# Kernel optimization log

Hardware: AMD Instinct MI355X
Metric: run time of the kernel (lower is better)

The kernel has to match this reference:

```python
import jax, jax.numpy as jnp
import numpy as np

N_NODES = 62      # config.note_num (SEED EEG electrodes)
BATCH   = 1024    # graphs per batch
IN_CH   = 5
HID     = 64
OUT_CH  = 3
K_HOPS  = 2       # config.K


def setup_inputs() -> dict:
    key = jax.random.key(0)
    ks = jax.random.split(key, 8)
    total = BATCH * N_NODES
    x = jax.random.normal(ks[0], (total, IN_CH), dtype=jnp.float32)
    # fully-connected per-graph edge_index in row-major order (incl. self-loops),
    # matching edge_weight.reshape(-1).repeat(batch_size) in the torch code
    src = jnp.repeat(jnp.arange(N_NODES, dtype=jnp.int32), N_NODES)
    dst = jnp.tile(jnp.arange(N_NODES, dtype=jnp.int32), N_NODES)
    offs = (jnp.arange(BATCH, dtype=jnp.int32) * N_NODES)[:, None]
    edge_index = jnp.stack([
        (src[None, :] + offs).reshape(-1),
        (dst[None, :] + offs).reshape(-1),
    ])  # [2, BATCH*3844]
    batch = jnp.repeat(jnp.arange(BATCH, dtype=jnp.int32), N_NODES)
    n_tril = N_NODES * (N_NODES + 1) // 2  # 1953
    edge_weight_param = jax.random.normal(ks[1], (n_tril,), dtype=jnp.float32)
    w1 = jax.random.normal(ks[2], (HID, IN_CH), dtype=jnp.float32) * (1.0 / np.sqrt(IN_CH))
    b1 = jnp.zeros((HID,), dtype=jnp.float32)
    w2 = jax.random.normal(ks[3], (HID, HID), dtype=jnp.float32) * (1.0 / np.sqrt(HID))
    b2 = jnp.zeros((HID,), dtype=jnp.float32)
    wfc = jax.random.normal(ks[4], (OUT_CH, HID), dtype=jnp.float32) * (1.0 / np.sqrt(HID))
    bfc = jnp.zeros((OUT_CH,), dtype=jnp.float32)
    return dict(x=x, edge_index=edge_index, batch=batch,
                edge_weight_param=edge_weight_param,
                w1=w1, b1=b1, w2=w2, b2=b2, wfc=wfc, bfc=bfc)


def _gcn_norm(edge_index, edge_weight, num_nodes):
    # Graph already contains every self-loop, so add_remaining_self_loops only
    # reorders edges; normalization math is identical on the original edge set.
    row, col = edge_index[0], edge_index[1]
    deg = jax.ops.segment_sum(jnp.abs(edge_weight), row, num_segments=num_nodes)
    deg_inv_sqrt = jnp.where(deg > 0, jax.lax.rsqrt(deg), 0.0)
    return deg_inv_sqrt[row] * edge_weight * deg_inv_sqrt[col]


def _rsgconv(x, src, dst, norm, w, b):
    n = x.shape[0]
    for _ in range(K_HOPS):  # K propagation hops (gather-scale-scatter)
        x = jax.ops.segment_sum(norm[:, None] * x[src], dst, num_segments=n)
    return x @ w.T + b


def reference(x, edge_index, batch, edge_weight_param, w1, b1, w2, b2, wfc, bfc):
    num_nodes = x.shape[0]
    # rebuild symmetric dense 62x62 edge-weight matrix from learnable tril vector
    xs, ys = jnp.tril_indices(N_NODES)
    W = jnp.zeros((N_NODES, N_NODES), dtype=x.dtype).at[xs, ys].set(edge_weight_param)
    W = W + W.T - jnp.diag(jnp.diag(W))
    edge_weight = jnp.tile(W.reshape(-1), BATCH)  # [BATCH*3844]
    norm = _gcn_norm(edge_index, edge_weight, num_nodes)
    src, dst = edge_index[0], edge_index[1]
    h = jax.nn.relu(_rsgconv(x, src, dst, norm, w1, b1))
    h = jax.nn.relu(_rsgconv(h, src, dst, norm, w2, b2))
    pooled = jax.ops.segment_sum(h, batch, num_segments=BATCH)  # global_add_pool
    # dropout is identity in eval mode
    return pooled @ wfc.T + bfc
```

## Files before the change

### kernel.cpp

```cpp
#include <hip/hip_runtime.h>

#define NN 62
#define NP 64
#define NBATCH 1024
#define IN_CH 5
#define HID 64
#define OUT_CH 3
#define NTRIL 1953
#define H1S 72
#define GS 17

typedef _Float16 f16;
typedef f16 half8 __attribute__((ext_vector_type(8)));
typedef float floatx4 __attribute__((ext_vector_type(4)));

__global__ __launch_bounds__(64) void setup_k(const float* __restrict__ p,
                                              const float* __restrict__ w2,
                                              f16* __restrict__ a2h,
                                              f16* __restrict__ a2l,
                                              f16* __restrict__ w2h,
                                              f16* __restrict__ w2l) {
    __shared__ float sA[NN * NP];
    __shared__ float sDinv[NN];
    const int lane = threadIdx.x;
    const int n = blockIdx.x;

    {
        float wv = w2[n * HID + lane];
        f16 wh = (f16)wv;
        w2h[n * NP + lane] = wh;
        w2l[n * NP + lane] = (f16)(wv - (float)wh);
    }

    for (int i = lane; i < NN * NP; i += 64) sA[i] = 0.f;
    __syncthreads();

    for (int i = lane; i < NTRIL; i += 64) {
        int r = (int)((sqrtf(8.f * (float)i + 1.f) - 1.f) * 0.5f);
        while (r * (r + 1) / 2 > i) --r;
        while ((r + 1) * (r + 2) / 2 <= i) ++r;
        int c = i - r * (r + 1) / 2;
        float v = p[i];
        sA[r * NP + c] = v;
        sA[c * NP + r] = v;
    }
    __syncthreads();

    if (lane < NN) {
        float s = 0.f;
        for (int j = 0; j < NN; ++j) s += fabsf(sA[lane * NP + j]);
        sDinv[lane] = (s > 0.f) ? (1.0f / sqrtf(s)) : 0.f;
    }
    __syncthreads();

    for (int i = lane; i < NN * NP; i += 64) {
        int r = i >> 6, c = i & 63;
        float dc = (c < NN) ? sDinv[c] : 0.f;
        sA[i] = sDinv[r] * sA[i] * dc;
    }
    __syncthreads();

    float acc = 0.f;
    if (n < NN)
        for (int k = 0; k < NN; ++k) acc += sA[n * NP + k] * sA[k * NP + lane];
    f16 ah = (f16)acc;
    a2h[n * NP + lane] = ah;
    a2l[n * NP + lane] = (f16)(acc - (float)ah);
}

__global__ __launch_bounds__(256, 4) void graph_net(
    const float* __restrict__ x,
    const f16* __restrict__ a2h, const f16* __restrict__ a2l,
    const f16* __restrict__ w2h, const f16* __restrict__ w2l,
    const float* __restrict__ w1, const float* __restrict__ b1,
    const float* __restrict__ b2,
    const float* __restrict__ wfc, const float* __restrict__ bfc,
    float* __restrict__ out) {
    __shared__ __align__(16) char smem[37120];
    f16* sUTh = (f16*)smem;
    f16* sUTl = (f16*)(smem + 9216);
    float* sG  = (float*)smem;
    f16* sH1h = (f16*)(smem + 18432);
    f16* sH1l = (f16*)(smem + 27648);
    float* sPool = (float*)(smem + 36864);

    const int t = threadIdx.x;
    const int lane = t & 63;
    const int w = __builtin_amdgcn_readfirstlane(t >> 6);
    const int g = blockIdx.x;
    const float* xg = x + (size_t)g * (NN * IN_CH);

    const int jn = lane & 15;
    const int qd = lane >> 4;
    const int jglob = 16 * w + jn;

    half8 aFh[4][2], aFl[4][2];
#pragma unroll
    for (int T = 0; T < 4; ++T)
#pragma unroll
        for (int ks = 0; ks < 2; ++ks) {
            aFh[T][ks] = *(const half8*)(a2h + (16 * T + jn) * NP + qd * 8 + 32 * ks);
            aFl[T][ks] = *(const half8*)(a2l + (16 * T + jn) * NP + qd * 8 + 32 * ks);
        }

    int xi[IN_CH];
    {
        const int L = (lane < NN) ? lane : (NN - 1);
        const int* xgi = (const int*)xg;
#pragma unroll
        for (int c = 0; c < IN_CH; ++c) xi[c] = xgi[L * IN_CH + c];
    }
    float w1r[IN_CH];
#pragma unroll
    for (int c = 0; c < IN_CH; ++c) w1r[c] = w1[lane * IN_CH + c];

#pragma unroll
    for (int ni = 0; ni < 16; ++ni) {
        const int n = 16 * w + ni;
        if (n < NN) {
            float u = 0.f;
#pragma unroll
            for (int c = 0; c < IN_CH; ++c)
                u += __int_as_float(__builtin_amdgcn_readlane(xi[c], n)) * w1r[c];
            f16 uh = (f16)u;
            sUTh[lane * H1S + n] = uh;
            sUTl[lane * H1S + n] = (f16)(u - (float)uh);
        }
    }
    if (t < 128) {
        const int n = 62 + (t >> 6);
        sUTh[(t & 63) * H1S + n] = (f16)0.f;
        sUTl[(t & 63) * H1S + n] = (f16)0.f;
    }
    __syncthreads();

    half8 bUh[2], bUl[2];
#pragma unroll
    for (int ks = 0; ks < 2; ++ks) {
        bUh[ks] = *(const half8*)(sUTh + jglob * H1S + qd * 8 + 32 * ks);
        bUl[ks] = *(const half8*)(sUTl + jglob * H1S + qd * 8 + 32 * ks);
    }
    floatx4 C1[4];
#pragma unroll
    for (int T = 0; T < 4; ++T) { C1[T][0]=0.f; C1[T][1]=0.f; C1[T][2]=0.f; C1[T][3]=0.f; }
#pragma unroll
    for (int T = 0; T < 4; ++T) {
#pragma unroll
        for (int ks = 0; ks < 2; ++ks) {
            C1[T] = __builtin_amdgcn_mfma_f32_16x16x32_f16(aFl[T][ks], bUh[ks], C1[T], 0, 0, 0);
            C1[T] = __builtin_amdgcn_mfma_f32_16x16x32_f16(aFh[T][ks], bUl[ks], C1[T], 0, 0, 0);
            C1[T] = __builtin_amdgcn_mfma_f32_16x16x32_f16(aFh[T][ks], bUh[ks], C1[T], 0, 0, 0);
        }
    }
    {
        const float b1r = b1[jglob];
#pragma unroll
        for (int T = 0; T < 4; ++T)
#pragma unroll
            for (int r = 0; r < 4; ++r) {
                const int n = 16 * T + qd * 4 + r;
                float v = fmaxf(C1[T][r] + b1r, 0.f);
                f16 vh = (f16)v;
                sH1h[n * H1S + jglob] = vh;
                sH1l[n * H1S + jglob] = (f16)(v - (float)vh);
            }
    }
    __syncthreads();

    half8 bWh[2], bWl[2];
#pragma unroll
    for (int ks = 0; ks < 2; ++ks) {
        bWh[ks] = *(const half8*)(w2h + jglob * NP + qd * 8 + 32 * ks);
        bWl[ks] = *(const half8*)(w2l + jglob * NP + qd * 8 + 32 * ks);
    }
    floatx4 Cg[4];
#pragma unroll
    for (int T = 0; T < 4; ++T) { Cg[T][0]=0.f; Cg[T][1]=0.f; Cg[T][2]=0.f; Cg[T][3]=0.f; }
#pragma unroll
    for (int T = 0; T < 4; ++T) {
#pragma unroll
        for (int ks = 0; ks < 2; ++ks) {
            const half8 aH = *(const half8*)(sH1h + (16 * T + jn) * H1S + qd * 8 + 32 * ks);
            const half8 aL = *(const half8*)(sH1l + (16 * T + jn) * H1S + qd * 8 + 32 * ks);
            Cg[T] = __builtin_amdgcn_mfma_f32_16x16x32_f16(aL, bWh[ks], Cg[T], 0, 0, 0);
            Cg[T] = __builtin_amdgcn_mfma_f32_16x16x32_f16(aH, bWl[ks], Cg[T], 0, 0, 0);
            Cg[T] = __builtin_amdgcn_mfma_f32_16x16x32_f16(aH, bWh[ks], Cg[T], 0, 0, 0);
        }
    }
    {
        float* gw = sG + w * (NP * GS);
#pragma unroll
        for (int T = 0; T < 4; ++T)
#pragma unroll
            for (int r = 0; r < 4; ++r)
                gw[(16 * T + qd * 4 + r) * GS + jn] = Cg[T][r];
    }
    __syncthreads();

    half8 bGh[2], bGl[2];
    {
        const float* gr = sG + w * (NP * GS);
#pragma unroll
        for (int ks = 0; ks < 2; ++ks)
#pragma unroll
            for (int i = 0; i < 8; ++i) {
                float v = gr[(qd * 8 + i + 32 * ks) * GS + jn];
                f16 vh = (f16)v;
                bGh[ks][i] = vh;
                bGl[ks][i] = (f16)(v - (float)vh);
            }
    }

    floatx4 C2[4];
#pragma unroll
    for (int T = 0; T < 4; ++T) { C2[T][0]=0.f; C2[T][1]=0.f; C2[T][2]=0.f; C2[T][3]=0.f; }
#pragma unroll
    for (int T = 0; T < 4; ++T) {
#pragma unroll
        for (int ks = 0; ks < 2; ++ks) {
            C2[T] = __builtin_amdgcn_mfma_f32_16x16x32_f16(aFl[T][ks], bGh[ks], C2[T], 0, 0, 0);
            C2[T] = __builtin_amdgcn_mfma_f32_16x16x32_f16(aFh[T][ks], bGl[ks], C2[T], 0, 0, 0);
            C2[T] = __builtin_amdgcn_mfma_f32_16x16x32_f16(aFh[T][ks], bGh[ks], C2[T], 0, 0, 0);
        }
    }

    {
        const float b2r = b2[jglob];
        float pool = 0.f;
#pragma unroll
        for (int T = 0; T < 4; ++T)
#pragma unroll
            for (int r = 0; r < 4; ++r) {
                const int n = 16 * T + qd * 4 + r;
                float v = fmaxf(C2[T][r] + b2r, 0.f);
                pool += (n < NN) ? v : 0.f;
            }
        pool += __shfl_xor(pool, 16);
        pool += __shfl_xor(pool, 32);
        if (lane < 16) sPool[jglob] = pool;
    }
    __syncthreads();

    if (t < OUT_CH) {
        float v = bfc[t];
        const float* wr = wfc + t * HID;
#pragma unroll
        for (int m = 0; m < HID; ++m) v += sPool[m] * wr[m];
        out[g * OUT_CH + t] = v;
    }
}

extern "C" void kernel_launch(void* const* d_in, const int* in_sizes, int n_in,
                              void* d_out, int out_size, void* d_ws, size_t ws_size,
                              hipStream_t stream) {
    const float* x   = (const float*)d_in[0];
    const float* ewp = (const float*)d_in[3];
    const float* w1  = (const float*)d_in[4];
    const float* b1  = (const float*)d_in[5];
    const float* w2  = (const float*)d_in[6];
    const float* b2  = (const float*)d_in[7];
    const float* wfc = (const float*)d_in[8];
    const float* bfc = (const float*)d_in[9];
    float* out = (float*)d_out;

    f16* a2h = (f16*)d_ws;
    f16* a2l = a2h + NP * NP;
    f16* w2h = a2l + NP * NP;
    f16* w2l = w2h + NP * NP;

    setup_k<<<NP, 64, 0, stream>>>(ewp, w2, a2h, a2l, w2h, w2l);
    graph_net<<<NBATCH, 256, 0, stream>>>(x, a2h, a2l, w2h, w2l,
                                          w1, b1, b2, wfc, bfc, out);
}
```

Baseline: 123.3 us.

## Compute first-layer x·W1 projection with MFMA and drop block-wide barriers

Replaces the scalar readlane-based x·W1ᵀ projection with split-f16 MFMA ops, for which W1 is pre-split into hi/lo halves in the setup kernel. The result goes through a per-wave shared-memory scratch region instead of a block-shared transpose buffer. Because each wave now only reads back its own slice, two __syncthreads barriers are removed and shared memory shrinks slightly. This adds 12 MFMAs that are mostly zero padding (K=5 padded to 32), in exchange for removing the serial readlane loop and the block synchronisation.

```diff
diff --git a/kernel.cpp b/kernel.cpp
--- a/kernel.cpp
+++ b/kernel.cpp
@@ -16,10 +16,13 @@
 
 __global__ __launch_bounds__(64) void setup_k(const float* __restrict__ p,
                                               const float* __restrict__ w2,
+                                              const float* __restrict__ w1,
                                               f16* __restrict__ a2h,
                                               f16* __restrict__ a2l,
                                               f16* __restrict__ w2h,
-                                              f16* __restrict__ w2l) {
+                                              f16* __restrict__ w2l,
+                                              f16* __restrict__ w1h,
+                                              f16* __restrict__ w1l) {
     __shared__ float sA[NN * NP];
     __shared__ float sDinv[NN];
     const int lane = threadIdx.x;
@@ -30,6 +33,12 @@
         f16 wh = (f16)wv;
         w2h[n * NP + lane] = wh;
         w2l[n * NP + lane] = (f16)(wv - (float)wh);
+    }
+    if (lane < 8) {
+        float wv = (lane < IN_CH) ? w1[n * IN_CH + lane] : 0.f;
+        f16 wh = (f16)wv;
+        w1h[n * 8 + lane] = wh;
+        w1l[n * 8 + lane] = (f16)(wv - (float)wh);
     }
 
     for (int i = lane; i < NN * NP; i += 64) sA[i] = 0.f;
@@ -72,17 +81,15 @@
     const float* __restrict__ x,
     const f16* __restrict__ a2h, const f16* __restrict__ a2l,
     const f16* __restrict__ w2h, const f16* __restrict__ w2l,
-    const float* __restrict__ w1, const float* __restrict__ b1,
-    const float* __restrict__ b2,
+    const f16* __restrict__ w1h, const f16* __restrict__ w1l,
+    const float* __restrict__ b1, const float* __restrict__ b2,
     const float* __restrict__ wfc, const float* __restrict__ bfc,
     float* __restrict__ out) {
-    __shared__ __align__(16) char smem[37120];
-    f16* sUTh = (f16*)smem;
-    f16* sUTl = (f16*)(smem + 9216);
-    float* sG  = (float*)smem;
-    f16* sH1h = (f16*)(smem + 18432);
-    f16* sH1l = (f16*)(smem + 27648);
-    float* sPool = (float*)(smem + 36864);
+    __shared__ __align__(16) char smem[36096];
+    float* sPG = (float*)smem;
+    f16* sH1h = (f16*)(smem + 17408);
+    f16* sH1l = (f16*)(smem + 26624);
+    float* sPool = (float*)(smem + 35840);
 
     const int t = threadIdx.x;
     const int lane = t & 63;
@@ -93,6 +100,7 @@
     const int jn = lane & 15;
     const int qd = lane >> 4;
     const int jglob = 16 * w + jn;
+    float* gw = sPG + w * (NP * GS);
 
     half8 aFh[4][2], aFl[4][2];
 #pragma unroll
@@ -103,43 +111,53 @@
             aFl[T][ks] = *(const half8*)(a2l + (16 * T + jn) * NP + qd * 8 + 32 * ks);
         }
 
-    int xi[IN_CH];
-    {
-        const int L = (lane < NN) ? lane : (NN - 1);
-        const int* xgi = (const int*)xg;
-#pragma unroll
-        for (int c = 0; c < IN_CH; ++c) xi[c] = xgi[L * IN_CH + c];
-    }
-    float w1r[IN_CH];
-#pragma unroll
-    for (int c = 0; c < IN_CH; ++c) w1r[c] = w1[lane * IN_CH + c];
-
-#pragma unroll
-    for (int ni = 0; ni < 16; ++ni) {
-        const int n = 16 * w + ni;
-        if (n < NN) {
-            float u = 0.f;
-#pragma unroll
-            for (int c = 0; c < IN_CH; ++c)
-                u += __int_as_float(__builtin_amdgcn_readlane(xi[c], n)) * w1r[c];
-            f16 uh = (f16)u;
-            sUTh[lane * H1S + n] = uh;
-            sUTl[lane * H1S + n] = (f16)(u - (float)uh);
-        }
-    }
-    if (t < 128) {
-        const int n = 62 + (t >> 6);
-        sUTh[(t & 63) * H1S + n] = (f16)0.f;
-        sUTl[(t & 63) * H1S + n] = (f16)0.f;
-    }
-    __syncthreads();
-
+    half8 aXh[4], aXl[4];
+#pragma unroll
+    for (int T = 0; T < 4; ++T) {
+        half8 hx = (half8)(f16)0.f, lx = (half8)(f16)0.f;
+        const int n = 16 * T + jn;
+        if (qd == 0 && n < NN) {
+            const float* xr = xg + n * IN_CH;
+#pragma unroll
+            for (int c = 0; c < IN_CH; ++c) {
+                float v = xr[c];
+                f16 vh = (f16)v;
+                hx[c] = vh;
+                lx[c] = (f16)(v - (float)vh);
+            }
+        }
+        aXh[T] = hx; aXl[T] = lx;
+    }
+    half8 bW1h = (half8)(f16)0.f, bW1l = (half8)(f16)0.f;
+    if (qd == 0) {
+        bW1h = *(const half8*)(w1h + jglob * 8);
+        bW1l = *(const half8*)(w1l + jglob * 8);
+    }
+    floatx4 P[4];
+#pragma unroll
+    for (int T = 0; T < 4; ++T) { P[T][0]=0.f; P[T][1]=0.f; P[T][2]=0.f; P[T][3]=0.f; }
+#pragma unroll
+    for (int T = 0; T < 4; ++T) {
+        P[T] = __builtin_amdgcn_mfma_f32_16x16x32_f16(aXl[T], bW1h, P[T], 0, 0, 0);
+        P[T] = __builtin_amdgcn_mfma_f32_16x16x32_f16(aXh[T], bW1l, P[T], 0, 0, 0);
+        P[T] = __builtin_amdgcn_mfma_f32_16x16x32_f16(aXh[T], bW1h, P[T], 0, 0, 0);
+    }
+#pragma unroll
+    for (int T = 0; T < 4; ++T)
+#pragma unroll
+        for (int r = 0; r < 4; ++r)
+            gw[(16 * T + qd * 4 + r) * GS + jn] = P[T][r];
     half8 bUh[2], bUl[2];
 #pragma unroll
-    for (int ks = 0; ks < 2; ++ks) {
-        bUh[ks] = *(const half8*)(sUTh + jglob * H1S + qd * 8 + 32 * ks);
-        bUl[ks] = *(const half8*)(sUTl + jglob * H1S + qd * 8 + 32 * ks);
-    }
+    for (int ks = 0; ks < 2; ++ks)
+#pragma unroll
+        for (int i = 0; i < 8; ++i) {
+            float v = gw[(qd * 8 + i + 32 * ks) * GS + jn];
+            f16 vh = (f16)v;
+            bUh[ks][i] = vh;
+            bUl[ks][i] = (f16)(v - (float)vh);
+        }
+
     floatx4 C1[4];
 #pragma unroll
     for (int T = 0; T < 4; ++T) { C1[T][0]=0.f; C1[T][1]=0.f; C1[T][2]=0.f; C1[T][3]=0.f; }
@@ -187,29 +205,21 @@
             Cg[T] = __builtin_amdgcn_mfma_f32_16x16x32_f16(aH, bWh[ks], Cg[T], 0, 0, 0);
         }
     }
-    {
-        float* gw = sG + w * (NP * GS);
-#pragma unroll
-        for (int T = 0; T < 4; ++T)
-#pragma unroll
-            for (int r = 0; r < 4; ++r)
-                gw[(16 * T + qd * 4 + r) * GS + jn] = Cg[T][r];
-    }
-    __syncthreads();
-
+#pragma unroll
+    for (int T = 0; T < 4; ++T)
+#pragma unroll
+        for (int r = 0; r < 4; ++r)
+            gw[(16 * T + qd * 4 + r) * GS + jn] = Cg[T][r];
     half8 bGh[2], bGl[2];
-    {
-        const float* gr = sG + w * (NP * GS);
-#pragma unroll
-        for (int ks = 0; ks < 2; ++ks)
-#pragma unroll
-            for (int i = 0; i < 8; ++i) {
-                float v = gr[(qd * 8 + i + 32 * ks) * GS + jn];
-                f16 vh = (f16)v;
-                bGh[ks][i] = vh;
-                bGl[ks][i] = (f16)(v - (float)vh);
-            }
-    }
+#pragma unroll
+    for (int ks = 0; ks < 2; ++ks)
+#pragma unroll
+        for (int i = 0; i < 8; ++i) {
+            float v = gw[(qd * 8 + i + 32 * ks) * GS + jn];
+            f16 vh = (f16)v;
+            bGh[ks][i] = vh;
+            bGl[ks][i] = (f16)(v - (float)vh);
+        }
 
     floatx4 C2[4];
 #pragma unroll
@@ -267,8 +277,10 @@
     f16* a2l = a2h + NP * NP;
     f16* w2h = a2l + NP * NP;
     f16* w2l = w2h + NP * NP;
-
-    setup_k<<<NP, 64, 0, stream>>>(ewp, w2, a2h, a2l, w2h, w2l);
-    graph_net<<<NBATCH, 256, 0, stream>>>(x, a2h, a2l, w2h, w2l,
-                                          w1, b1, b2, wfc, bfc, out);
+    f16* w1h = w2l + NP * NP;
+    f16* w1l = w1h + NP * 8;
+
+    setup_k<<<NP, 64, 0, stream>>>(ewp, w2, w1, a2h, a2l, w2h, w2l, w1h, w1l);
+    graph_net<<<NBATCH, 256, 0, stream>>>(x, a2h, a2l, w2h, w2l, w1h, w1l,
+                                          b1, b2, wfc, bfc, out);
 }
```

Measured after the change: 124.3 us. Within noise of the previous version (+0.9%).
